# Optimization experiments

Measured on AMD Instinct MI355X. Metric: run time of the kernel, lower is better.

## Reference

```python
import jax, jax.numpy as jnp
import numpy as np

B, H, L, DH = 4, 16, 2048, 64
EMBED_DIM = H * DH
CAUSAL = True


def setup_inputs() -> dict:
    key = jax.random.key(0)
    kq, kk, kv = jax.random.split(key, 3)
    return {
        "query": jax.random.normal(kq, (B, H, L, DH), dtype=jnp.float32),
        "key": jax.random.normal(kk, (B, H, L, DH), dtype=jnp.float32),
        "value": jax.random.normal(kv, (B, H, L, DH), dtype=jnp.float32),
    }


def reference(query, key, value):
    # scaled dot-product attention with causal mask, inputs [B, H, L, Dh]
    scale = 1.0 / jnp.sqrt(jnp.asarray(query.shape[-1], query.dtype))
    scores = jnp.einsum("bhld,bhsd->bhls", query, key) * scale  # [B,H,L,S]
    if CAUSAL:
        q_idx = jnp.arange(query.shape[-2])[:, None]
        k_idx = jnp.arange(key.shape[-2])[None, :]
        neg_inf = jnp.asarray(-jnp.inf, scores.dtype)
        scores = jnp.where(k_idx > q_idx, neg_inf, scores)
    attn = jax.nn.softmax(scores, axis=-1)
    out = jnp.einsum("bhls,bhsd->bhld", attn, value)  # [B,H,L,Dh]
    # merge heads -> [B, L, D]
    b = out.shape[0]
    return out.transpose(0, 2, 1, 3).reshape(b, -1, EMBED_DIM)
```

## Files before the change

kernel.cpp:

```cpp
#include <hip/hip_runtime.h>
#include <hip/hip_bf16.h>

#define B_   4
#define H_   16
#define L_   2048
#define DH_  64
#define QSCALE 0.1803368801111204f
#define LDK  72

typedef __bf16 bf16;
typedef __bf16 bf16x4 __attribute__((ext_vector_type(4)));
typedef __bf16 bf16x8 __attribute__((ext_vector_type(8)));
typedef float  f32x4  __attribute__((ext_vector_type(4)));

typedef const __attribute__((address_space(1))) unsigned int* gptr_t;
typedef __attribute__((address_space(3))) unsigned int* lptr_t;

__device__ __forceinline__ void load_lds16(const bf16* g, bf16* l) {
    __builtin_amdgcn_global_load_lds((gptr_t)(const void*)g, (lptr_t)(void*)l, 16, 0, 0);
}

__global__ __launch_bounds__(256, 4)
void prep(const float* __restrict__ K, const float* __restrict__ V,
          bf16* __restrict__ Kb, bf16* __restrict__ Vtg)
{
    __shared__ bf16 tl[64 * 72];
    const int t   = threadIdx.x;
    const int r   = t >> 2;
    const int c4  = t & 3;
    const int bid = blockIdx.x;
    const int kt  = bid & 31;
    const int bh  = bid >> 5;

    const float* Kp = K + ((size_t)bh * L_ + kt * 64) * DH_;
    const float* Vp = V + ((size_t)bh * L_ + kt * 64) * DH_;
    bf16* Kbp = Kb  + (size_t)bh * (L_ * DH_) + (size_t)(kt * 64) * DH_;
    bf16* Vtp = Vtg + (size_t)bh * (DH_ * L_) + kt * 64;

    {
        const float* src = Kp + r * DH_ + c4 * 16;
        f32x4 a = *(const f32x4*)(src);
        f32x4 b = *(const f32x4*)(src + 4);
        f32x4 c = *(const f32x4*)(src + 8);
        f32x4 d = *(const f32x4*)(src + 12);
        bf16x8 lo, hi;
        #pragma unroll
        for (int j = 0; j < 4; ++j) {
            lo[j] = (bf16)a[j]; lo[j + 4] = (bf16)b[j];
            hi[j] = (bf16)c[j]; hi[j + 4] = (bf16)d[j];
        }
        const int b0 = 2 * c4, b1 = 2 * c4 + 1;
        *(bf16x8*)(Kbp + r * 64 + (b0 ^ (r & 7)) * 8) = lo;
        *(bf16x8*)(Kbp + r * 64 + (b1 ^ (r & 7)) * 8) = hi;
    }
    {
        const float* src = Vp + r * DH_ + c4 * 16;
        f32x4 a = *(const f32x4*)(src);
        f32x4 b = *(const f32x4*)(src + 4);
        f32x4 c = *(const f32x4*)(src + 8);
        f32x4 d = *(const f32x4*)(src + 12);
        #pragma unroll
        for (int j = 0; j < 4; ++j) {
            tl[(c4 * 16 + j)      * 72 + r] = (bf16)a[j];
            tl[(c4 * 16 + 4 + j)  * 72 + r] = (bf16)b[j];
            tl[(c4 * 16 + 8 + j)  * 72 + r] = (bf16)c[j];
            tl[(c4 * 16 + 12 + j) * 72 + r] = (bf16)d[j];
        }
    }
    __syncthreads();
    {
        const int d = r;
        #pragma unroll
        for (int bi = 0; bi < 2; ++bi) {
            const int blk = 2 * c4 + bi;
            bf16x8 v;
            #pragma unroll
            for (int j = 0; j < 8; ++j) v[j] = tl[d * 72 + blk * 8 + j];
            *(bf16x8*)(Vtp + (size_t)d * L_ + (blk ^ (d & 7)) * 8) = v;
        }
    }
}

__global__ __launch_bounds__(256, 2)
void fa_fwd3(const float* __restrict__ Q, const bf16* __restrict__ Kb,
             const bf16* __restrict__ Vtg, float* __restrict__ O)
{
    __shared__ __align__(16) bf16 smem[2][2][64 * 64];
    __shared__ __align__(16) bf16 Pl[4][16 * 64];

    const int tid  = threadIdx.x;
    const int wave = tid >> 6;
    const int lane = tid & 63;
    const int quad = lane >> 4;
    const int l15  = lane & 15;

    const int u    = blockIdx.x;
    const int xcd  = u & 7;
    const int t    = u >> 3;
    const int bh   = xcd * 8 + (t & 7);
    const int pidx = t >> 3;

    const int h    = bh & 15;
    const int b    = bh >> 4;

    const float* Qbh = Q + (size_t)bh * L_ * DH_;
    const bf16* Kbh  = Kb  + (size_t)bh * (L_ * DH_);
    const bf16* Vbh  = Vtg + (size_t)bh * (DH_ * L_);

    const int Rw = 16 * wave;
    const int lr = lane >> 3;
    const int lb = lane & 7;

    bf16x8 vone;
    #pragma unroll
    for (int jj = 0; jj < 8; ++jj) vone[jj] = (bf16)1.0f;

    int swb[2];
    #pragma unroll
    for (int ss = 0; ss < 2; ++ss) swb[ss] = ((4 * ss + quad) ^ (l15 & 7)) * 8;

    for (int pass = 0; pass < 2; ++pass) {
        const int Qt   = pass ? (15 - pidx) : pidx;
        const int q0   = Qt * 128;
        const int jmax = 2 * Qt + 1;

        bf16x8 qf[2][2];
        #pragma unroll
        for (int qg = 0; qg < 2; ++qg) {
            const int row = q0 + 32 * wave + 16 * qg + l15;
            const float* qp = Qbh + (size_t)row * DH_ + quad * 8;
            #pragma unroll
            for (int ss = 0; ss < 2; ++ss) {
                f32x4 a = *(const f32x4*)(qp + ss * 32);
                f32x4 c = *(const f32x4*)(qp + ss * 32 + 4);
                #pragma unroll
                for (int jj = 0; jj < 4; ++jj) {
                    qf[qg][ss][jj]     = (bf16)(a[jj] * QSCALE);
                    qf[qg][ss][jj + 4] = (bf16)(c[jj] * QSCALE);
                }
            }
        }

        f32x4 o_acc[2][4];
        f32x4 l_acc[2];
        #pragma unroll
        for (int qg = 0; qg < 2; ++qg) {
            l_acc[qg] = (f32x4)0.0f;
            #pragma unroll
            for (int ct = 0; ct < 4; ++ct) o_acc[qg][ct] = (f32x4)0.0f;
        }

        bf16x8 pa[2][2];
        bf16x8 bvp[4][2];

        {
            const bf16* kg = Kbh + (size_t)(Rw + lr) * 64 + lb * 8;
            const bf16* vg = Vbh + (size_t)(Rw + lr) * L_ + lb * 8;
            bf16* kl = &smem[0][0][Rw * 64];
            bf16* vl = &smem[0][1][Rw * 64];
            load_lds16(kg, kl);              load_lds16(kg + 8 * 64, kl + 8 * 64);
            load_lds16(vg, vl);              load_lds16(vg + (size_t)8 * L_, vl + 8 * 64);
        }

        for (int j = 0; j <= jmax; ++j) {
            __syncthreads();
            const int cur = j & 1;

            if (j < jmax) {
                const int nb  = cur ^ 1;
                const int kv0 = (j + 1) * 64;
                const bf16* kg = Kbh + (size_t)(kv0 + Rw + lr) * 64 + lb * 8;
                const bf16* vg = Vbh + (size_t)(Rw + lr) * L_ + kv0 + lb * 8;
                bf16* kl = &smem[nb][0][Rw * 64];
                bf16* vl = &smem[nb][1][Rw * 64];
                load_lds16(kg, kl);          load_lds16(kg + 8 * 64, kl + 8 * 64);
                load_lds16(vg, vl);          load_lds16(vg + (size_t)8 * L_, vl + 8 * 64);
            }

            const bf16* Kl = smem[cur][0];
            const bf16* Vt = smem[cur][1];

            bf16x8 bk[4][2];
            #pragma unroll
            for (int ct = 0; ct < 4; ++ct)
                #pragma unroll
                for (int ss = 0; ss < 2; ++ss)
                    bk[ct][ss] = *(const bf16x8*)&Kl[(16 * ct + l15) * 64 + swb[ss]];

            if (j > 0) {
                __builtin_amdgcn_s_setprio(1);
                #pragma unroll
                for (int ct = 0; ct < 4; ++ct)
                    #pragma unroll
                    for (int ss = 0; ss < 2; ++ss)
                        #pragma unroll
                        for (int qg = 0; qg < 2; ++qg)
                            o_acc[qg][ct] = __builtin_amdgcn_mfma_f32_16x16x32_bf16(pa[qg][ss], bvp[ct][ss], o_acc[qg][ct], 0, 0, 0);
                #pragma unroll
                for (int qg = 0; qg < 2; ++qg)
                    #pragma unroll
                    for (int ss = 0; ss < 2; ++ss)
                        l_acc[qg] = __builtin_amdgcn_mfma_f32_16x16x32_bf16(pa[qg][ss], vone, l_acc[qg], 0, 0, 0);
                __builtin_amdgcn_s_setprio(0);
            }

            #pragma unroll
            for (int ct = 0; ct < 4; ++ct)
                #pragma unroll
                for (int ss = 0; ss < 2; ++ss)
                    bvp[ct][ss] = *(const bf16x8*)&Vt[(16 * ct + l15) * 64 + swb[ss]];

            #pragma unroll
            for (int qg = 0; qg < 2; ++qg) {
                f32x4 sacc[4];
                #pragma unroll
                for (int ct = 0; ct < 4; ++ct) {
                    f32x4 acc = (f32x4)0.0f;
                    #pragma unroll
                    for (int ss = 0; ss < 2; ++ss)
                        acc = __builtin_amdgcn_mfma_f32_16x16x32_bf16(bk[ct][ss], qf[qg][ss], acc, 0, 0, 0);
                    sacc[ct] = acc;
                }

                if (j >= 2 * Qt) {
                    const int rlim = 32 * wave + 16 * qg + l15 - ((j - 2 * Qt) << 6);
                    #pragma unroll
                    for (int ct = 0; ct < 4; ++ct) {
                        #pragma unroll
                        for (int r = 0; r < 4; ++r)
                            if (16 * ct + quad * 4 + r > rlim) sacc[ct][r] = -1e30f;
                    }
                }

                #pragma unroll
                for (int ct = 0; ct < 4; ++ct) {
                    bf16x4 pk;
                    #pragma unroll
                    for (int r = 0; r < 4; ++r) pk[r] = (bf16)exp2f(sacc[ct][r]);
                    const int blk = 2 * ct + (quad >> 1);
                    *(bf16x4*)&Pl[wave][l15 * 64 + ((blk ^ (l15 & 7)) * 8) + (quad & 1) * 4] = pk;
                }
                #pragma unroll
                for (int ss = 0; ss < 2; ++ss)
                    pa[qg][ss] = *(const bf16x8*)&Pl[wave][l15 * 64 + swb[ss]];
            }
        }

        __builtin_amdgcn_s_setprio(1);
        #pragma unroll
        for (int ct = 0; ct < 4; ++ct)
            #pragma unroll
            for (int ss = 0; ss < 2; ++ss)
                #pragma unroll
                for (int qg = 0; qg < 2; ++qg)
                    o_acc[qg][ct] = __builtin_amdgcn_mfma_f32_16x16x32_bf16(pa[qg][ss], bvp[ct][ss], o_acc[qg][ct], 0, 0, 0);
        #pragma unroll
        for (int qg = 0; qg < 2; ++qg)
            #pragma unroll
            for (int ss = 0; ss < 2; ++ss)
                l_acc[qg] = __builtin_amdgcn_mfma_f32_16x16x32_bf16(pa[qg][ss], vone, l_acc[qg], 0, 0, 0);
        __builtin_amdgcn_s_setprio(0);

        __syncthreads();

        #pragma unroll
        for (int qg = 0; qg < 2; ++qg)
            #pragma unroll
            for (int r = 0; r < 4; ++r) {
                const float inv = 1.0f / l_acc[qg][r];
                const int qrow = q0 + 32 * wave + 16 * qg + quad * 4 + r;
                float* op = &O[((size_t)b * L_ + qrow) * (H_ * DH_) + h * DH_];
                #pragma unroll
                for (int ct = 0; ct < 4; ++ct)
                    op[16 * ct + l15] = o_acc[qg][ct][r] * inv;
            }
    }
}

__global__ __launch_bounds__(256, 4)
void fa_fwd(const float* __restrict__ Q, const float* __restrict__ K,
            const float* __restrict__ V, float* __restrict__ O)
{
    __shared__ __align__(16) bf16 Kl[64 * LDK];
    __shared__ __align__(16) bf16 Vt[64 * LDK];
    __shared__ __align__(16) bf16 Pl[4][16 * LDK];

    const int tid  = threadIdx.x;
    const int wave = tid >> 6;
    const int lane = tid & 63;
    const int quad = lane >> 4;
    const int l15  = lane & 15;

    const int u    = blockIdx.x;
    const int xcd  = u & 7;
    const int p    = u >> 3;
    const int bh   = xcd * 8 + (p & 7);
    const int pidx = p >> 3;
    const int h    = bh & 15;
    const int b    = bh >> 4;

    const float* Qbh = Q + (size_t)bh * L_ * DH_;
    const float* Kbh = K + (size_t)bh * L_ * DH_;
    const float* Vbh = V + (size_t)bh * L_ * DH_;

    const int r0 = tid >> 4;
    const int c0 = (tid & 15) * 4;

    for (int pass = 0; pass < 2; ++pass) {
        const int qt = pass ? (31 - pidx) : pidx;
        const int q0 = qt * 64;

        bf16x8 qf[2];
        {
            const int row = q0 + wave * 16 + l15;
            const float* qp = Qbh + (size_t)row * DH_ + quad * 8;
            #pragma unroll
            for (int s = 0; s < 2; ++s) {
                f32x4 a = *(const f32x4*)(qp + s * 32);
                f32x4 c = *(const f32x4*)(qp + s * 32 + 4);
                #pragma unroll
                for (int jj = 0; jj < 4; ++jj) {
                    qf[s][jj]     = (bf16)(a[jj] * QSCALE);
                    qf[s][jj + 4] = (bf16)(c[jj] * QSCALE);
                }
            }
        }

        float m_run[4], l_run[4];
        f32x4 o_acc[4];
        #pragma unroll
        for (int r = 0; r < 4; ++r) { m_run[r] = -1e30f; l_run[r] = 0.0f; }
        #pragma unroll
        for (int ct = 0; ct < 4; ++ct) o_acc[ct] = (f32x4)0.0f;

        f32x4 kreg[4], vreg[4];
        #pragma unroll
        for (int i = 0; i < 4; ++i) {
            kreg[i] = *(const f32x4*)(Kbh + (size_t)(r0 + 16 * i) * DH_ + c0);
            vreg[i] = *(const f32x4*)(Vbh + (size_t)(r0 + 16 * i) * DH_ + c0);
        }

        for (int j = 0; j <= qt; ++j) {
            __syncthreads();
            #pragma unroll
            for (int i = 0; i < 4; ++i) {
                const int row = r0 + 16 * i;
                bf16x4 kb;
                #pragma unroll
                for (int c = 0; c < 4; ++c) kb[c] = (bf16)kreg[i][c];
                *(bf16x4*)&Kl[row * LDK + c0] = kb;
                Vt[(c0 + 0) * LDK + row] = (bf16)vreg[i][0];
                Vt[(c0 + 1) * LDK + row] = (bf16)vreg[i][1];
                Vt[(c0 + 2) * LDK + row] = (bf16)vreg[i][2];
                Vt[(c0 + 3) * LDK + row] = (bf16)vreg[i][3];
            }
            __syncthreads();

            if (j < qt) {
                const int kv0 = (j + 1) * 64;
                #pragma unroll
                for (int i = 0; i < 4; ++i) {
                    kreg[i] = *(const f32x4*)(Kbh + (size_t)(kv0 + r0 + 16 * i) * DH_ + c0);
                    vreg[i] = *(const f32x4*)(Vbh + (size_t)(kv0 + r0 + 16 * i) * DH_ + c0);
                }
            }

            f32x4 sacc[4];
            #pragma unroll
            for (int ct = 0; ct < 4; ++ct) {
                f32x4 acc = (f32x4)0.0f;
                #pragma unroll
                for (int s = 0; s < 2; ++s) {
                    bf16x8 bk = *(const bf16x8*)&Kl[(16 * ct + l15) * LDK + 32 * s + quad * 8];
                    acc = __builtin_amdgcn_mfma_f32_16x16x32_bf16(qf[s], bk, acc, 0, 0, 0);
                }
                sacc[ct] = acc;
            }

            if (j == qt) {
                #pragma unroll
                for (int ct = 0; ct < 4; ++ct) {
                    const int keyl = 16 * ct + l15;
                    #pragma unroll
                    for (int r = 0; r < 4; ++r)
                        if (keyl > wave * 16 + quad * 4 + r) sacc[ct][r] = -1e30f;
                }
            }

            #pragma unroll
            for (int r = 0; r < 4; ++r) {
                float mx = fmaxf(fmaxf(sacc[0][r], sacc[1][r]), fmaxf(sacc[2][r], sacc[3][r]));
                mx = fmaxf(mx, __shfl_xor(mx, 1));
                mx = fmaxf(mx, __shfl_xor(mx, 2));
                mx = fmaxf(mx, __shfl_xor(mx, 4));
                mx = fmaxf(mx, __shfl_xor(mx, 8));
                const float mnew  = fmaxf(m_run[r], mx);
                const float alpha = exp2f(m_run[r] - mnew);
                float sum = 0.0f;
                #pragma unroll
                for (int ct = 0; ct < 4; ++ct) {
                    const float pv = exp2f(sacc[ct][r] - mnew);
                    sacc[ct][r] = pv;
                    sum += pv;
                }
                sum += __shfl_xor(sum, 1);
                sum += __shfl_xor(sum, 2);
                sum += __shfl_xor(sum, 4);
                sum += __shfl_xor(sum, 8);
                l_run[r] = l_run[r] * alpha + sum;
                m_run[r] = mnew;
                #pragma unroll
                for (int ct = 0; ct < 4; ++ct) o_acc[ct][r] *= alpha;
            }

            #pragma unroll
            for (int ct = 0; ct < 4; ++ct)
                #pragma unroll
                for (int r = 0; r < 4; ++r)
                    Pl[wave][(quad * 4 + r) * LDK + 16 * ct + l15] = (bf16)sacc[ct][r];

            bf16x8 pa[2];
            #pragma unroll
            for (int s = 0; s < 2; ++s)
                pa[s] = *(const bf16x8*)&Pl[wave][l15 * LDK + 32 * s + quad * 8];

            #pragma unroll
            for (int ct = 0; ct < 4; ++ct)
                #pragma unroll
                for (int s = 0; s < 2; ++s) {
                    bf16x8 bv = *(const bf16x8*)&Vt[(16 * ct + l15) * LDK + 32 * s + quad * 8];
                    o_acc[ct] = __builtin_amdgcn_mfma_f32_16x16x32_bf16(pa[s], bv, o_acc[ct], 0, 0, 0);
                }
        }

        #pragma unroll
        for (int ct = 0; ct < 4; ++ct)
            #pragma unroll
            for (int r = 0; r < 4; ++r) {
                const int qrow = q0 + wave * 16 + quad * 4 + r;
                O[((size_t)b * L_ + qrow) * (H_ * DH_) + h * DH_ + (16 * ct + l15)] =
                    o_acc[ct][r] / l_run[r];
            }
    }
}

extern "C" void kernel_launch(void* const* d_in, const int* in_sizes, int n_in,
                              void* d_out, int out_size, void* d_ws, size_t ws_size,
                              hipStream_t stream) {
    const float* q = (const float*)d_in[0];
    const float* k = (const float*)d_in[1];
    const float* v = (const float*)d_in[2];
    float* out = (float*)d_out;
    const size_t need = 2ull * (size_t)(B_ * H_) * L_ * DH_ * sizeof(bf16);
    if (ws_size >= need) {
        bf16* Kb  = (bf16*)d_ws;
        bf16* Vtg = Kb + (size_t)(B_ * H_) * L_ * DH_;
        prep<<<dim3(B_ * H_ * (L_ / 64)), dim3(256), 0, stream>>>(k, v, Kb, Vtg);
        fa_fwd3<<<dim3(512), dim3(256), 0, stream>>>(q, Kb, Vtg, out);
    } else {
        fa_fwd<<<dim3(B_ * H_ * 16), dim3(256), 0, stream>>>(q, k, v, out);
    }
}
```

Measured before the change: 190.8 us.

## Read K/V tiles directly from global memory, dropping LDS double buffering

```diff
diff --git a/kernel.cpp b/kernel.cpp
--- a/kernel.cpp
+++ b/kernel.cpp
@@ -12,13 +12,6 @@
 typedef __bf16 bf16x4 __attribute__((ext_vector_type(4)));
 typedef __bf16 bf16x8 __attribute__((ext_vector_type(8)));
 typedef float  f32x4  __attribute__((ext_vector_type(4)));
-
-typedef const __attribute__((address_space(1))) unsigned int* gptr_t;
-typedef __attribute__((address_space(3))) unsigned int* lptr_t;
-
-__device__ __forceinline__ void load_lds16(const bf16* g, bf16* l) {
-    __builtin_amdgcn_global_load_lds((gptr_t)(const void*)g, (lptr_t)(void*)l, 16, 0, 0);
-}
 
 __global__ __launch_bounds__(256, 4)
 void prep(const float* __restrict__ K, const float* __restrict__ V,
@@ -85,7 +78,6 @@
 void fa_fwd3(const float* __restrict__ Q, const bf16* __restrict__ Kb,
              const bf16* __restrict__ Vtg, float* __restrict__ O)
 {
-    __shared__ __align__(16) bf16 smem[2][2][64 * 64];
     __shared__ __align__(16) bf16 Pl[4][16 * 64];
 
     const int tid  = threadIdx.x;
@@ -107,10 +99,6 @@
     const bf16* Kbh  = Kb  + (size_t)bh * (L_ * DH_);
     const bf16* Vbh  = Vtg + (size_t)bh * (DH_ * L_);
 
-    const int Rw = 16 * wave;
-    const int lr = lane >> 3;
-    const int lb = lane & 7;
-
     bf16x8 vone;
     #pragma unroll
     for (int jj = 0; jj < 8; ++jj) vone[jj] = (bf16)1.0f;
@@ -150,66 +138,28 @@
             for (int ct = 0; ct < 4; ++ct) o_acc[qg][ct] = (f32x4)0.0f;
         }
 
-        bf16x8 pa[2][2];
-        bf16x8 bvp[4][2];
-
-        {
-            const bf16* kg = Kbh + (size_t)(Rw + lr) * 64 + lb * 8;
-            const bf16* vg = Vbh + (size_t)(Rw + lr) * L_ + lb * 8;
-            bf16* kl = &smem[0][0][Rw * 64];
-            bf16* vl = &smem[0][1][Rw * 64];
-            load_lds16(kg, kl);              load_lds16(kg + 8 * 64, kl + 8 * 64);
-            load_lds16(vg, vl);              load_lds16(vg + (size_t)8 * L_, vl + 8 * 64);
-        }
-
         for (int j = 0; j <= jmax; ++j) {
-            __syncthreads();
-            const int cur = j & 1;
-
-            if (j < jmax) {
-                const int nb  = cur ^ 1;
-                const int kv0 = (j + 1) * 64;
-                const bf16* kg = Kbh + (size_t)(kv0 + Rw + lr) * 64 + lb * 8;
-                const bf16* vg = Vbh + (size_t)(Rw + lr) * L_ + kv0 + lb * 8;
-                bf16* kl = &smem[nb][0][Rw * 64];
-                bf16* vl = &smem[nb][1][Rw * 64];
-                load_lds16(kg, kl);          load_lds16(kg + 8 * 64, kl + 8 * 64);
-                load_lds16(vg, vl);          load_lds16(vg + (size_t)8 * L_, vl + 8 * 64);
-            }
-
-            const bf16* Kl = smem[cur][0];
-            const bf16* Vt = smem[cur][1];
+            const bool active = (j < 2 * Qt) || ((32 * wave + 31) >= ((j - 2 * Qt) << 6));
+            if (!active) continue;
+
+            const int kv0 = j * 64;
+            const bf16* Kt = Kbh + (size_t)kv0 * 64;
 
             bf16x8 bk[4][2];
             #pragma unroll
             for (int ct = 0; ct < 4; ++ct)
                 #pragma unroll
                 for (int ss = 0; ss < 2; ++ss)
-                    bk[ct][ss] = *(const bf16x8*)&Kl[(16 * ct + l15) * 64 + swb[ss]];
-
-            if (j > 0) {
-                __builtin_amdgcn_s_setprio(1);
-                #pragma unroll
-                for (int ct = 0; ct < 4; ++ct)
-                    #pragma unroll
-                    for (int ss = 0; ss < 2; ++ss)
-                        #pragma unroll
-                        for (int qg = 0; qg < 2; ++qg)
-                            o_acc[qg][ct] = __builtin_amdgcn_mfma_f32_16x16x32_bf16(pa[qg][ss], bvp[ct][ss], o_acc[qg][ct], 0, 0, 0);
-                #pragma unroll
-                for (int qg = 0; qg < 2; ++qg)
-                    #pragma unroll
-                    for (int ss = 0; ss < 2; ++ss)
-                        l_acc[qg] = __builtin_amdgcn_mfma_f32_16x16x32_bf16(pa[qg][ss], vone, l_acc[qg], 0, 0, 0);
-                __builtin_amdgcn_s_setprio(0);
-            }
-
+                    bk[ct][ss] = *(const bf16x8*)&Kt[(16 * ct + l15) * 64 + swb[ss]];
+
+            bf16x8 bv[4][2];
             #pragma unroll
             for (int ct = 0; ct < 4; ++ct)
                 #pragma unroll
                 for (int ss = 0; ss < 2; ++ss)
-                    bvp[ct][ss] = *(const bf16x8*)&Vt[(16 * ct + l15) * 64 + swb[ss]];
-
+                    bv[ct][ss] = *(const bf16x8*)&Vbh[(size_t)(16 * ct + l15) * L_ + kv0 + swb[ss]];
+
+            bf16x8 pa[2][2];
             #pragma unroll
             for (int qg = 0; qg < 2; ++qg) {
                 f32x4 sacc[4];
@@ -244,24 +194,22 @@
                 for (int ss = 0; ss < 2; ++ss)
                     pa[qg][ss] = *(const bf16x8*)&Pl[wave][l15 * 64 + swb[ss]];
             }
-        }
-
-        __builtin_amdgcn_s_setprio(1);
-        #pragma unroll
-        for (int ct = 0; ct < 4; ++ct)
-            #pragma unroll
-            for (int ss = 0; ss < 2; ++ss)
-                #pragma unroll
-                for (int qg = 0; qg < 2; ++qg)
-                    o_acc[qg][ct] = __builtin_amdgcn_mfma_f32_16x16x32_bf16(pa[qg][ss], bvp[ct][ss], o_acc[qg][ct], 0, 0, 0);
-        #pragma unroll
-        for (int qg = 0; qg < 2; ++qg)
-            #pragma unroll
-            for (int ss = 0; ss < 2; ++ss)
-                l_acc[qg] = __builtin_amdgcn_mfma_f32_16x16x32_bf16(pa[qg][ss], vone, l_acc[qg], 0, 0, 0);
-        __builtin_amdgcn_s_setprio(0);
-
-        __syncthreads();
+
+            __builtin_amdgcn_s_setprio(1);
+            #pragma unroll
+            for (int ct = 0; ct < 4; ++ct)
+                #pragma unroll
+                for (int ss = 0; ss < 2; ++ss)
+                    #pragma unroll
+                    for (int qg = 0; qg < 2; ++qg)
+                        o_acc[qg][ct] = __builtin_amdgcn_mfma_f32_16x16x32_bf16(pa[qg][ss], bv[ct][ss], o_acc[qg][ct], 0, 0, 0);
+            #pragma unroll
+            for (int qg = 0; qg < 2; ++qg)
+                #pragma unroll
+                for (int ss = 0; ss < 2; ++ss)
+                    l_acc[qg] = __builtin_amdgcn_mfma_f32_16x16x32_bf16(pa[qg][ss], vone, l_acc[qg], 0, 0, 0);
+            __builtin_amdgcn_s_setprio(0);
+        }
 
         #pragma unroll
         for (int qg = 0; qg < 2; ++qg)
```

Measured after the change: 195.6 us. 1.02x slower.
